# Kernel tuning notes

Measured on AMD Instinct MI355X. Metric: run time of the kernel, lower is better.

## Reference

```python
import jax, jax.numpy as jnp
import numpy as np

B, N, DIM = 4, 2048, 1024
H, DH = 16, 64


def setup_inputs() -> dict:
    key = jax.random.key(0)
    k1, k2, k3 = jax.random.split(key, 3)
    x = jax.random.normal(k1, (B, N, DIM), dtype=jnp.float32)
    # nn.Linear weight layout: [out_features, in_features]; y = x @ W.T
    w_qkv = jax.random.normal(k2, (3 * H * DH, DIM), dtype=jnp.float32) * (DIM ** -0.5)
    w_out = jax.random.normal(k3, (DIM, H * DH), dtype=jnp.float32) * ((H * DH) ** -0.5)
    b_out = jnp.zeros((DIM,), dtype=jnp.float32)
    return {"x": x, "w_qkv": w_qkv, "w_out": w_out, "b_out": b_out}


def reference(x, w_qkv, w_out, b_out):
    scale = DH ** -0.5
    qkv = jnp.einsum('bnd,ed->bne', x, w_qkv)            # [B,N,3*H*DH]
    q, k, v = jnp.split(qkv, 3, axis=-1)
    def to_heads(t):
        return t.reshape(B, N, H, DH).transpose(0, 2, 1, 3)  # b h n d
    q, k, v = to_heads(q), to_heads(k), to_heads(v)
    scores = jnp.einsum('bhnd,bhmd->bhnm', q, k) * scale  # [B,H,N,N]
    att = jax.nn.softmax(scores, axis=-1)
    out = jnp.einsum('bhnm,bhmd->bhnd', att, v)
    out = out.transpose(0, 2, 1, 3).reshape(B, N, H * DH)  # b n (h d)
    return jnp.einsum('bne,de->bnd', out, w_out) + b_out
```

## Files before the change

kernel.cpp:

```cpp
#include <hip/hip_runtime.h>
#include <hip/hip_bf16.h>
#include <math.h>

#define B_   4
#define N_   2048
#define DIM_ 1024
#define H_   16
#define DH_  64
#define E3_  3072

typedef __attribute__((ext_vector_type(8)))  short s8v;
typedef __attribute__((ext_vector_type(4)))  float f4v;
typedef __attribute__((ext_vector_type(16))) float f16v;

__device__ __forceinline__ unsigned short f2bf_fast(float f) {
    return (unsigned short)((__builtin_bit_cast(unsigned int, f) + 0x8000u) >> 16);
}
__device__ __forceinline__ unsigned int pkbf(float a, float b) {
    unsigned int ua = __builtin_bit_cast(unsigned int, a) + 0x8000u;
    unsigned int ub = __builtin_bit_cast(unsigned int, b) + 0x8000u;
    return __builtin_amdgcn_perm(ub, ua, 0x07060302);
}
__device__ __forceinline__ unsigned int cvtpk(float a, float b) {
    unsigned int r;
    asm("v_cvt_pk_bf16_f32 %0, %1, %2" : "=v"(r) : "v"(a), "v"(b));
    return r;
}
__device__ __forceinline__ uint2 pl32(unsigned int a, unsigned int b) {
    asm volatile("v_permlane32_swap_b32 %0, %1" : "+v"(a), "+v"(b));
    return make_uint2(a, b);
}

__device__ __forceinline__ void gload_lds16(const void* g, void* l) {
    __builtin_amdgcn_global_load_lds(
        (const __attribute__((address_space(1))) unsigned int*)(uintptr_t)g,
        (__attribute__((address_space(3))) unsigned int*)(uintptr_t)l,
        16, 0, 0);
}

__global__ __launch_bounds__(256) void cvt_bf16(
    const float* __restrict__ in, unsigned short* __restrict__ out, int n)
{
    const int i = (blockIdx.x * 256 + threadIdx.x) * 4;
    if (i < n) {
        float4 v = *(const float4*)(in + i);
        uint2 pk;
        pk.x = pkbf(v.x, v.y);
        pk.y = pkbf(v.z, v.w);
        *(uint2*)(out + i) = pk;
    }
}

__global__ __launch_bounds__(512, 1) void gemm_qkv(
    const unsigned short* __restrict__ A,
    const unsigned short* __restrict__ Bw,
    unsigned short* __restrict__ Cb,
    unsigned short* __restrict__ Vt)
{
    __shared__ unsigned short Ls[2][28672];

    const int tid  = threadIdx.x;
    const int w    = tid >> 6;
    const int lane = tid & 63;
    const int quad = lane >> 4;
    const int l15  = lane & 15;
    const int wm   = w & 1;
    const int wn   = w >> 1;

    const int lin = blockIdx.y * 16 + blockIdx.x;
    const int swz = (lin & 7) * 64 + (lin >> 3);
    const int m0  = (swz >> 4) * 256;
    const int n0  = (swz & 15) * 192;

    const int r8  = lane >> 3;
    const int chk = (lane & 7) ^ r8;

    f4v acc[8][3];
    #pragma unroll
    for (int i = 0; i < 8; i++)
        #pragma unroll
        for (int j = 0; j < 3; j++) acc[i][j] = (f4v){0.f, 0.f, 0.f, 0.f};

    #pragma unroll
    for (int j = 0; j < 7; j++) {
        const int u = w * 7 + j;
        const unsigned short* src = (u < 32)
            ? A  + (size_t)(m0 + u * 8 + r8) * 1024 + chk * 8
            : Bw + (size_t)(n0 + (u - 32) * 8 + r8) * 1024 + chk * 8;
        gload_lds16(src, &Ls[0][u * 512]);
    }
    __syncthreads();

    for (int t = 0; t < 16; t++) {
        const int cur = t & 1;

        if (t + 1 < 16) {
            const int k0 = (t + 1) * 64;
            #pragma unroll
            for (int j = 0; j < 7; j++) {
                const int u = w * 7 + j;
                const unsigned short* src = (u < 32)
                    ? A  + (size_t)(m0 + u * 8 + r8) * 1024 + k0 + chk * 8
                    : Bw + (size_t)(n0 + (u - 32) * 8 + r8) * 1024 + k0 + chk * 8;
                gload_lds16(src, &Ls[cur ^ 1][u * 512]);
            }
        }

        #pragma unroll
        for (int s = 0; s < 2; s++) {
            s8v af[8], bf[3];
            #pragma unroll
            for (int ms = 0; ms < 8; ms++) {
                const int row = wm * 128 + ms * 16 + l15;
                af[ms] = *(const s8v*)&Ls[cur][row * 64 + (((s * 4 + quad) ^ (l15 & 7)) * 8)];
            }
            #pragma unroll
            for (int ns = 0; ns < 3; ns++) {
                const int row = 256 + wn * 48 + ns * 16 + l15;
                bf[ns] = *(const s8v*)&Ls[cur][row * 64 + (((s * 4 + quad) ^ (l15 & 7)) * 8)];
            }
            __builtin_amdgcn_s_setprio(1);
            #pragma unroll
            for (int ms = 0; ms < 8; ms++)
                #pragma unroll
                for (int ns = 0; ns < 3; ns++)
                    acc[ms][ns] = __builtin_amdgcn_mfma_f32_16x16x32_bf16(
                        af[ms], bf[ns], acc[ms][ns], 0, 0, 0);
            __builtin_amdgcn_s_setprio(0);
        }

        __syncthreads();
    }

    #pragma unroll
    for (int ns = 0; ns < 3; ns++) {
        const int colb = n0 + wn * 48 + ns * 16;
        if (colb < 2048) {
            const float mul = (colb < 1024) ? 0.18033688011112042f : 1.0f;
            #pragma unroll
            for (int ms = 0; ms < 8; ms++)
                #pragma unroll
                for (int r = 0; r < 4; r++) {
                    const int row = m0 + wm * 128 + ms * 16 + quad * 4 + r;
                    Cb[(size_t)row * E3_ + colb + l15] = f2bf_fast(acc[ms][ns][r] * mul);
                }
        } else {
            const int e = colb + l15 - 2048;
            const int hh = e >> 6, d = e & 63;
            #pragma unroll
            for (int ms = 0; ms < 8; ms++) {
                const int row = m0 + wm * 128 + ms * 16 + quad * 4;
                const int bb = row >> 11, nn = row & 2047;
                uint2 pk;
                pk.x = pkbf(acc[ms][ns][0], acc[ms][ns][1]);
                pk.y = pkbf(acc[ms][ns][2], acc[ms][ns][3]);
                *(uint2*)&Vt[(((size_t)bb * 16 + hh) * 64 + d) * 2048 + nn] = pk;
            }
        }
    }
}

__global__ __launch_bounds__(256) void gemm_out(
    const unsigned short* __restrict__ A,
    const unsigned short* __restrict__ Bw,
    const float* __restrict__ bias,
    float* __restrict__ Cf,
    int M, int Nc, int K)
{
    __shared__ unsigned short As[128 * 32];
    __shared__ unsigned short Bs[128 * 32];

    const int tid  = threadIdx.x;
    const int w    = tid >> 6;
    const int lane = tid & 63;
    const int quad = lane >> 4;
    const int l15  = lane & 15;
    const int wm   = w & 1, wn = w >> 1;

    const int nwx = gridDim.x;
    const int lin = blockIdx.y * nwx + blockIdx.x;
    const int cpx = (nwx * gridDim.y) >> 3;
    const int swz = (lin & 7) * cpx + (lin >> 3);
    const int m0  = (swz / nwx) * 128, n0 = (swz % nwx) * 128;

    const int srow = lane >> 2;
    const int sch  = (lane & 3) * 8;

    f4v acc[4][4];
    #pragma unroll
    for (int i = 0; i < 4; i++)
        #pragma unroll
        for (int j = 0; j < 4; j++) acc[i][j] = (f4v){0.f, 0.f, 0.f, 0.f};

    for (int k0 = 0; k0 < K; k0 += 32) {
        __syncthreads();
        #pragma unroll
        for (int i = 0; i < 2; i++) {
            const int rbase = w * 32 + i * 16;
            gload_lds16(A  + (size_t)(m0 + rbase + srow) * K + k0 + sch,
                        &As[rbase * 32]);
            gload_lds16(Bw + (size_t)(n0 + rbase + srow) * K + k0 + sch,
                        &Bs[rbase * 32]);
        }
        __syncthreads();

        s8v af[4], bf[4];
        #pragma unroll
        for (int i = 0; i < 4; i++) {
            af[i] = *(const s8v*)&As[(wm * 64 + i * 16 + l15) * 32 + quad * 8];
            bf[i] = *(const s8v*)&Bs[(wn * 64 + i * 16 + l15) * 32 + quad * 8];
        }
        #pragma unroll
        for (int ms = 0; ms < 4; ms++)
            #pragma unroll
            for (int ns = 0; ns < 4; ns++)
                acc[ms][ns] = __builtin_amdgcn_mfma_f32_16x16x32_bf16(
                    af[ms], bf[ns], acc[ms][ns], 0, 0, 0);
    }

    #pragma unroll
    for (int ns = 0; ns < 4; ns++) {
        const float bz = bias[n0 + wn * 64 + ns * 16 + l15];
        #pragma unroll
        for (int ms = 0; ms < 4; ms++)
            #pragma unroll
            for (int r = 0; r < 4; r++) {
                const int row = m0 + wm * 64 + ms * 16 + quad * 4 + r;
                Cf[(size_t)row * Nc + n0 + wn * 64 + ns * 16 + l15] =
                    acc[ms][ns][r] + bz;
            }
    }
}

__global__ __launch_bounds__(512, 4) void attn_mfma(
    const unsigned short* __restrict__ qkv,
    const unsigned short* __restrict__ vT,
    unsigned short* __restrict__ ao)
{
    __shared__ __align__(16) unsigned short Ks[2][64][64];
    __shared__ __align__(16) unsigned short Vs[2][64][64];

    const int tid  = threadIdx.x;
    const int w    = tid >> 6;
    const int lane = tid & 63;
    const int l31  = lane & 31;
    const int hi5  = lane >> 5;
    const int h8   = hi5 * 8;

    const int lin = blockIdx.y * 8 + blockIdx.x;
    const int swz = (lin & 7) * 64 + (lin >> 3);
    const int bx  = swz & 7;
    const int bh  = swz >> 3;
    const int b   = bh >> 4;
    const int h   = bh & 15;
    const int q0  = bx * 256;
    const int qb  = q0 + w * 32;

    const unsigned short* qp  = qkv + (size_t)b * N_ * E3_ + (size_t)h * DH_;
    const unsigned short* kp  = qp + 1024;
    const unsigned short* vtp = vT + (size_t)bh * 64 * 2048;

    const int drow = lane >> 3;
    const int dchk = (lane & 7) ^ drow;
    const int grow = w * 8 + drow;

    s8v bq[4];
    {
        const unsigned short* qrow = qp + (size_t)(qb + l31) * E3_;
        #pragma unroll
        for (int ks = 0; ks < 4; ks++)
            bq[ks] = *(const s8v*)(qrow + ks * 16 + h8);
    }

    s8v ones;
    #pragma unroll
    for (int i = 0; i < 8; i++) ones[i] = (short)0x3F80;

    const f16v fzero = {0.f,0.f,0.f,0.f,0.f,0.f,0.f,0.f,
                        0.f,0.f,0.f,0.f,0.f,0.f,0.f,0.f};
    f16v o0 = fzero, o1 = fzero;
    f16v lc = fzero;

    gload_lds16(kp  + (size_t)grow * E3_  + dchk * 8, &Ks[0][w * 8][0]);
    gload_lds16(vtp + (size_t)grow * 2048 + dchk * 8, &Vs[0][w * 8][0]);
    __syncthreads();

    for (int kt = 0; kt < N_ / 64; kt++) {
        const int cur = kt & 1;

        if (kt + 1 < N_ / 64) {
            const int kn = (kt + 1) * 64;
            gload_lds16(kp  + (size_t)(kn + grow) * E3_  + dchk * 8,
                        &Ks[cur ^ 1][w * 8][0]);
            gload_lds16(vtp + (size_t)grow * 2048 + kn + dchk * 8,
                        &Vs[cur ^ 1][w * 8][0]);
        }

        #pragma unroll
        for (int ksub = 0; ksub < 2; ksub++) {
            const int krow = ksub * 32 + l31;
            const int ksw  = (l31 & 7) * 8;
            s8v ak[4];
            #pragma unroll
            for (int ks = 0; ks < 4; ks++)
                ak[ks] = *(const s8v*)&Ks[cur][krow][(ks * 16 + h8) ^ ksw];

            f16v st = fzero;
            __builtin_amdgcn_s_setprio(1);
            st = __builtin_amdgcn_mfma_f32_32x32x16_bf16(ak[0], bq[0], st, 0, 0, 0);
            st = __builtin_amdgcn_mfma_f32_32x32x16_bf16(ak[1], bq[1], st, 0, 0, 0);
            st = __builtin_amdgcn_mfma_f32_32x32x16_bf16(ak[2], bq[2], st, 0, 0, 0);
            st = __builtin_amdgcn_mfma_f32_32x32x16_bf16(ak[3], bq[3], st, 0, 0, 0);
            __builtin_amdgcn_s_setprio(0);

            float pe[16];
            #pragma unroll
            for (int i = 0; i < 16; i++)
                pe[i] = __builtin_amdgcn_exp2f(st[i]);

            s8v pa[2];
            {
                union { s8v v; unsigned int u[4]; } f0, f1;
                uint2 r;
                r = pl32(cvtpk(pe[0],  pe[1]),  cvtpk(pe[4],  pe[5]));
                f0.u[0] = r.x; f0.u[2] = r.y;
                r = pl32(cvtpk(pe[2],  pe[3]),  cvtpk(pe[6],  pe[7]));
                f0.u[1] = r.x; f0.u[3] = r.y;
                r = pl32(cvtpk(pe[8],  pe[9]),  cvtpk(pe[12], pe[13]));
                f1.u[0] = r.x; f1.u[2] = r.y;
                r = pl32(cvtpk(pe[10], pe[11]), cvtpk(pe[14], pe[15]));
                f1.u[1] = r.x; f1.u[3] = r.y;
                pa[0] = f0.v;
                pa[1] = f1.v;
            }

            #pragma unroll
            for (int j = 0; j < 2; j++) {
                const int kbase = (ksub * 2 + j) * 16 + h8;
                const int vsw   = (l31 & 7) * 8;
                s8v bv0 = *(const s8v*)&Vs[cur][l31     ][kbase ^ vsw];
                s8v bv1 = *(const s8v*)&Vs[cur][32 + l31][kbase ^ vsw];
                __builtin_amdgcn_s_setprio(1);
                o0 = __builtin_amdgcn_mfma_f32_32x32x16_bf16(pa[j], bv0, o0, 0, 0, 0);
                o1 = __builtin_amdgcn_mfma_f32_32x32x16_bf16(pa[j], bv1, o1, 0, 0, 0);
                lc = __builtin_amdgcn_mfma_f32_32x32x16_bf16(pa[j], ones, lc, 0, 0, 0);
                __builtin_amdgcn_s_setprio(0);
            }
        }

        __syncthreads();
    }

    {
        float inv[16];
        #pragma unroll
        for (int r = 0; r < 16; r++) inv[r] = 1.f / lc[r];
        #pragma unroll
        for (int r = 0; r < 16; r++) {
            const int qrow = qb + (r & 3) + 8 * (r >> 2) + 4 * hi5;
            const size_t base = ((size_t)b * N_ + qrow) * (H_ * DH_) + h * DH_;
            ao[base + l31]      = f2bf_fast(o0[r] * inv[r]);
            ao[base + 32 + l31] = f2bf_fast(o1[r] * inv[r]);
        }
    }
}

extern "C" void kernel_launch(void* const* d_in, const int* in_sizes, int n_in,
                              void* d_out, int out_size, void* d_ws, size_t ws_size,
                              hipStream_t stream) {
    const float* x     = (const float*)d_in[0];
    const float* w_qkv = (const float*)d_in[1];
    const float* w_out = (const float*)d_in[2];
    const float* b_out = (const float*)d_in[3];
    float* out = (float*)d_out;

    char* ws = (char*)d_ws;
    unsigned short* x_bf    = (unsigned short*)(ws);
    unsigned short* wqkv_bf = (unsigned short*)(ws + (((size_t)16) << 20));
    unsigned short* wout_bf = (unsigned short*)(ws + (((size_t)22) << 20));
    unsigned short* qkv_bf  = (unsigned short*)(ws + (((size_t)24) << 20));
    unsigned short* vT      = (unsigned short*)(ws + (((size_t)72) << 20));
    unsigned short* ao_bf   = (unsigned short*)(ws + (((size_t)88) << 20));

    const int M = B_ * N_;

    cvt_bf16<<<(M * DIM_) / 1024, 256, 0, stream>>>(x, x_bf, M * DIM_);
    cvt_bf16<<<(E3_ * DIM_) / 1024, 256, 0, stream>>>(w_qkv, wqkv_bf, E3_ * DIM_);
    cvt_bf16<<<(DIM_ * DIM_) / 1024, 256, 0, stream>>>(w_out, wout_bf, DIM_ * DIM_);

    {
        dim3 grid(E3_ / 192, M / 256);
        gemm_qkv<<<grid, 512, 0, stream>>>(x_bf, wqkv_bf, qkv_bf, vT);
    }
    {
        dim3 grid(N_ / 256, B_ * H_);
        attn_mfma<<<grid, 512, 0, stream>>>(qkv_bf, vT, ao_bf);
    }
    {
        dim3 grid(DIM_ / 128, M / 128);
        gemm_out<<<grid, 256, 0, stream>>>(ao_bf, wout_bf, b_out,
                                           out, M, DIM_, DIM_);
    }
    (void)in_sizes; (void)n_in; (void)out_size; (void)ws_size;
}
```

Baseline: 257.7 us.

## Process two query sub-tiles per wave in attention to reuse K/V fragments

Each wave now handles 64 query rows (two 32-row sub-tiles) instead of 32, so every K and V fragment read from LDS feeds twice as many MFMAs. Each block covers 512 queries, the grid is halved, the block swizzle is adjusted, and launch bounds drop to 2 blocks per CU to allow more registers. This cuts LDS reads and global K/V tile loads per unit of work. The cost is higher register pressure, lower occupancy, and fewer blocks (256) to spread across the CUs.

```diff
diff --git a/kernel.cpp b/kernel.cpp
--- a/kernel.cpp
+++ b/kernel.cpp
@@ -232,7 +232,7 @@
     }
 }
 
-__global__ __launch_bounds__(512, 4) void attn_mfma(
+__global__ __launch_bounds__(512, 2) void attn_mfma(
     const unsigned short* __restrict__ qkv,
     const unsigned short* __restrict__ vT,
     unsigned short* __restrict__ ao)
@@ -247,14 +247,13 @@
     const int hi5  = lane >> 5;
     const int h8   = hi5 * 8;
 
-    const int lin = blockIdx.y * 8 + blockIdx.x;
-    const int swz = (lin & 7) * 64 + (lin >> 3);
-    const int bx  = swz & 7;
-    const int bh  = swz >> 3;
+    const int lin = blockIdx.y * 4 + blockIdx.x;
+    const int j0  = (lin & 7) * 32 + (lin >> 3);
+    const int bx  = j0 & 3;
+    const int bh  = j0 >> 2;
     const int b   = bh >> 4;
     const int h   = bh & 15;
-    const int q0  = bx * 256;
-    const int qb  = q0 + w * 32;
+    const int qb  = bx * 512 + w * 64;
 
     const unsigned short* qp  = qkv + (size_t)b * N_ * E3_ + (size_t)h * DH_;
     const unsigned short* kp  = qp + 1024;
@@ -264,12 +263,13 @@
     const int dchk = (lane & 7) ^ drow;
     const int grow = w * 8 + drow;
 
-    s8v bq[4];
-    {
-        const unsigned short* qrow = qp + (size_t)(qb + l31) * E3_;
+    s8v bq[2][4];
+    #pragma unroll
+    for (int sub = 0; sub < 2; sub++) {
+        const unsigned short* qrow = qp + (size_t)(qb + sub * 32 + l31) * E3_;
         #pragma unroll
         for (int ks = 0; ks < 4; ks++)
-            bq[ks] = *(const s8v*)(qrow + ks * 16 + h8);
+            bq[sub][ks] = *(const s8v*)(qrow + ks * 16 + h8);
     }
 
     s8v ones;
@@ -278,8 +278,10 @@
 
     const f16v fzero = {0.f,0.f,0.f,0.f,0.f,0.f,0.f,0.f,
                         0.f,0.f,0.f,0.f,0.f,0.f,0.f,0.f};
-    f16v o0 = fzero, o1 = fzero;
-    f16v lc = fzero;
+    f16v o[2][2];
+    o[0][0] = fzero; o[0][1] = fzero; o[1][0] = fzero; o[1][1] = fzero;
+    f16v lc[2];
+    lc[0] = fzero; lc[1] = fzero;
 
     gload_lds16(kp  + (size_t)grow * E3_  + dchk * 8, &Ks[0][w * 8][0]);
     gload_lds16(vtp + (size_t)grow * 2048 + dchk * 8, &Vs[0][w * 8][0]);
@@ -305,21 +307,22 @@
             for (int ks = 0; ks < 4; ks++)
                 ak[ks] = *(const s8v*)&Ks[cur][krow][(ks * 16 + h8) ^ ksw];
 
-            f16v st = fzero;
-            __builtin_amdgcn_s_setprio(1);
-            st = __builtin_amdgcn_mfma_f32_32x32x16_bf16(ak[0], bq[0], st, 0, 0, 0);
-            st = __builtin_amdgcn_mfma_f32_32x32x16_bf16(ak[1], bq[1], st, 0, 0, 0);
-            st = __builtin_amdgcn_mfma_f32_32x32x16_bf16(ak[2], bq[2], st, 0, 0, 0);
-            st = __builtin_amdgcn_mfma_f32_32x32x16_bf16(ak[3], bq[3], st, 0, 0, 0);
-            __builtin_amdgcn_s_setprio(0);
-
-            float pe[16];
-            #pragma unroll
-            for (int i = 0; i < 16; i++)
-                pe[i] = __builtin_amdgcn_exp2f(st[i]);
-
-            s8v pa[2];
-            {
+            s8v pa[2][2];
+            #pragma unroll
+            for (int sub = 0; sub < 2; sub++) {
+                f16v st = fzero;
+                __builtin_amdgcn_s_setprio(1);
+                st = __builtin_amdgcn_mfma_f32_32x32x16_bf16(ak[0], bq[sub][0], st, 0, 0, 0);
+                st = __builtin_amdgcn_mfma_f32_32x32x16_bf16(ak[1], bq[sub][1], st, 0, 0, 0);
+                st = __builtin_amdgcn_mfma_f32_32x32x16_bf16(ak[2], bq[sub][2], st, 0, 0, 0);
+                st = __builtin_amdgcn_mfma_f32_32x32x16_bf16(ak[3], bq[sub][3], st, 0, 0, 0);
+                __builtin_amdgcn_s_setprio(0);
+
+                float pe[16];
+                #pragma unroll
+                for (int i = 0; i < 16; i++)
+                    pe[i] = __builtin_amdgcn_exp2f(st[i]);
+
                 union { s8v v; unsigned int u[4]; } f0, f1;
                 uint2 r;
                 r = pl32(cvtpk(pe[0],  pe[1]),  cvtpk(pe[4],  pe[5]));
@@ -330,8 +333,8 @@
                 f1.u[0] = r.x; f1.u[2] = r.y;
                 r = pl32(cvtpk(pe[10], pe[11]), cvtpk(pe[14], pe[15]));
                 f1.u[1] = r.x; f1.u[3] = r.y;
-                pa[0] = f0.v;
-                pa[1] = f1.v;
+                pa[sub][0] = f0.v;
+                pa[sub][1] = f1.v;
             }
 
             #pragma unroll
@@ -341,9 +344,12 @@
                 s8v bv0 = *(const s8v*)&Vs[cur][l31     ][kbase ^ vsw];
                 s8v bv1 = *(const s8v*)&Vs[cur][32 + l31][kbase ^ vsw];
                 __builtin_amdgcn_s_setprio(1);
-                o0 = __builtin_amdgcn_mfma_f32_32x32x16_bf16(pa[j], bv0, o0, 0, 0, 0);
-                o1 = __builtin_amdgcn_mfma_f32_32x32x16_bf16(pa[j], bv1, o1, 0, 0, 0);
-                lc = __builtin_amdgcn_mfma_f32_32x32x16_bf16(pa[j], ones, lc, 0, 0, 0);
+                o[0][0] = __builtin_amdgcn_mfma_f32_32x32x16_bf16(pa[0][j], bv0, o[0][0], 0, 0, 0);
+                o[0][1] = __builtin_amdgcn_mfma_f32_32x32x16_bf16(pa[0][j], bv1, o[0][1], 0, 0, 0);
+                o[1][0] = __builtin_amdgcn_mfma_f32_32x32x16_bf16(pa[1][j], bv0, o[1][0], 0, 0, 0);
+                o[1][1] = __builtin_amdgcn_mfma_f32_32x32x16_bf16(pa[1][j], bv1, o[1][1], 0, 0, 0);
+                lc[0]   = __builtin_amdgcn_mfma_f32_32x32x16_bf16(pa[0][j], ones, lc[0], 0, 0, 0);
+                lc[1]   = __builtin_amdgcn_mfma_f32_32x32x16_bf16(pa[1][j], ones, lc[1], 0, 0, 0);
                 __builtin_amdgcn_s_setprio(0);
             }
         }
@@ -351,16 +357,18 @@
         __syncthreads();
     }
 
-    {
+    #pragma unroll
+    for (int sub = 0; sub < 2; sub++) {
         float inv[16];
         #pragma unroll
-        for (int r = 0; r < 16; r++) inv[r] = 1.f / lc[r];
+        for (int r = 0; r < 16; r++) inv[r] = 1.f / lc[sub][r];
         #pragma unroll
         for (int r = 0; r < 16; r++) {
-            const int qrow = qb + (r & 3) + 8 * (r >> 2) + 4 * hi5;
+            const int crow = (r & 3) + 8 * (r >> 2) + 4 * hi5;
+            const int qrow = qb + sub * 32 + crow;
             const size_t base = ((size_t)b * N_ + qrow) * (H_ * DH_) + h * DH_;
-            ao[base + l31]      = f2bf_fast(o0[r] * inv[r]);
-            ao[base + 32 + l31] = f2bf_fast(o1[r] * inv[r]);
+            ao[base + l31]      = f2bf_fast(o[sub][0][r] * inv[r]);
+            ao[base + 32 + l31] = f2bf_fast(o[sub][1][r] * inv[r]);
         }
     }
 }
@@ -393,7 +401,7 @@
         gemm_qkv<<<grid, 512, 0, stream>>>(x_bf, wqkv_bf, qkv_bf, vT);
     }
     {
-        dim3 grid(N_ / 256, B_ * H_);
+        dim3 grid(N_ / 512, B_ * H_);
         attn_mfma<<<grid, 512, 0, stream>>>(qkv_bf, vT, ao_bf);
     }
     {
```

After: 254.3 us. About the same (-1.3%).

## Double-buffer and swizzle the output GEMM, and fuse the bf16 conversion launches

Applied to the files above, without the earlier changes.

The output-projection GEMM now uses a K-tile of 64 with two LDS buffers, so the next tile's global-to-LDS load overlaps the current tile's MFMAs. It also XOR-swizzles the LDS chunks to avoid bank conflicts and raises wave priority around the MFMA block. The three fp32-to-bf16 conversion launches are merged into one kernel to cut launch overhead. Shapes are now hardcoded, and the larger LDS footprint may limit how many blocks fit per CU.

```diff
diff --git a/kernel.cpp b/kernel.cpp
--- a/kernel.cpp
+++ b/kernel.cpp
@@ -38,17 +38,23 @@
         16, 0, 0);
 }
 
-__global__ __launch_bounds__(256) void cvt_bf16(
-    const float* __restrict__ in, unsigned short* __restrict__ out, int n)
+__global__ __launch_bounds__(256) void cvt_all(
+    const float* __restrict__ x,  const float* __restrict__ wq,
+    const float* __restrict__ wo,
+    unsigned short* __restrict__ xb, unsigned short* __restrict__ wqb,
+    unsigned short* __restrict__ wob)
 {
-    const int i = (blockIdx.x * 256 + threadIdx.x) * 4;
-    if (i < n) {
-        float4 v = *(const float4*)(in + i);
-        uint2 pk;
-        pk.x = pkbf(v.x, v.y);
-        pk.y = pkbf(v.z, v.w);
-        *(uint2*)(out + i) = pk;
-    }
+    const int bid = blockIdx.x;
+    const float* in; unsigned short* out; int rb;
+    if (bid < 8192)       { in = x;  out = xb;  rb = bid; }
+    else if (bid < 11264) { in = wq; out = wqb; rb = bid - 8192; }
+    else                  { in = wo; out = wob; rb = bid - 11264; }
+    const int i = (rb * 256 + threadIdx.x) * 4;
+    float4 v = *(const float4*)(in + i);
+    uint2 pk;
+    pk.x = pkbf(v.x, v.y);
+    pk.y = pkbf(v.z, v.w);
+    *(uint2*)(out + i) = pk;
 }
 
 __global__ __launch_bounds__(512, 1) void gemm_qkv(
@@ -160,31 +166,29 @@
     }
 }
 
-__global__ __launch_bounds__(256) void gemm_out(
+__global__ __launch_bounds__(256, 2) void gemm_out(
     const unsigned short* __restrict__ A,
     const unsigned short* __restrict__ Bw,
     const float* __restrict__ bias,
-    float* __restrict__ Cf,
-    int M, int Nc, int K)
+    float* __restrict__ Cf)
 {
-    __shared__ unsigned short As[128 * 32];
-    __shared__ unsigned short Bs[128 * 32];
+    __shared__ unsigned short Ls[2][16384];
 
     const int tid  = threadIdx.x;
     const int w    = tid >> 6;
     const int lane = tid & 63;
     const int quad = lane >> 4;
     const int l15  = lane & 15;
-    const int wm   = w & 1, wn = w >> 1;
-
-    const int nwx = gridDim.x;
-    const int lin = blockIdx.y * nwx + blockIdx.x;
-    const int cpx = (nwx * gridDim.y) >> 3;
-    const int swz = (lin & 7) * cpx + (lin >> 3);
-    const int m0  = (swz / nwx) * 128, n0 = (swz % nwx) * 128;
-
-    const int srow = lane >> 2;
-    const int sch  = (lane & 3) * 8;
+    const int wm   = w & 1;
+    const int wn   = w >> 1;
+
+    const int lin = blockIdx.y * 8 + blockIdx.x;
+    const int swz = (lin & 7) * 64 + (lin >> 3);
+    const int m0  = (swz >> 3) * 128;
+    const int n0  = (swz & 7) * 128;
+
+    const int r8  = lane >> 3;
+    const int chk = (lane & 7) ^ r8;
 
     f4v acc[4][4];
     #pragma unroll
@@ -192,30 +196,55 @@
         #pragma unroll
         for (int j = 0; j < 4; j++) acc[i][j] = (f4v){0.f, 0.f, 0.f, 0.f};
 
-    for (int k0 = 0; k0 < K; k0 += 32) {
+    #pragma unroll
+    for (int j = 0; j < 8; j++) {
+        const int u = w * 8 + j;
+        const unsigned short* src = (u < 16)
+            ? A  + (size_t)(m0 + u * 8 + r8) * 1024 + chk * 8
+            : Bw + (size_t)(n0 + (u - 16) * 8 + r8) * 1024 + chk * 8;
+        gload_lds16(src, &Ls[0][u * 512]);
+    }
+    __syncthreads();
+
+    for (int t = 0; t < 16; t++) {
+        const int cur = t & 1;
+
+        if (t + 1 < 16) {
+            const int k0 = (t + 1) * 64;
+            #pragma unroll
+            for (int j = 0; j < 8; j++) {
+                const int u = w * 8 + j;
+                const unsigned short* src = (u < 16)
+                    ? A  + (size_t)(m0 + u * 8 + r8) * 1024 + k0 + chk * 8
+                    : Bw + (size_t)(n0 + (u - 16) * 8 + r8) * 1024 + k0 + chk * 8;
+                gload_lds16(src, &Ls[cur ^ 1][u * 512]);
+            }
+        }
+
+        #pragma unroll
+        for (int s = 0; s < 2; s++) {
+            s8v af[4], bf[4];
+            #pragma unroll
+            for (int ms = 0; ms < 4; ms++) {
+                const int row = wm * 64 + ms * 16 + l15;
+                af[ms] = *(const s8v*)&Ls[cur][row * 64 + (((s * 4 + quad) ^ (l15 & 7)) * 8)];
+            }
+            #pragma unroll
+            for (int ns = 0; ns < 4; ns++) {
+                const int row = 128 + wn * 64 + ns * 16 + l15;
+                bf[ns] = *(const s8v*)&Ls[cur][row * 64 + (((s * 4 + quad) ^ (l15 & 7)) * 8)];
+            }
+            __builtin_amdgcn_s_setprio(1);
+            #pragma unroll
+            for (int ms = 0; ms < 4; ms++)
+                #pragma unroll
+                for (int ns = 0; ns < 4; ns++)
+                    acc[ms][ns] = __builtin_amdgcn_mfma_f32_16x16x32_bf16(
+                        af[ms], bf[ns], acc[ms][ns], 0, 0, 0);
+            __builtin_amdgcn_s_setprio(0);
+        }
+
         __syncthreads();
-        #pragma unroll
-        for (int i = 0; i < 2; i++) {
-            const int rbase = w * 32 + i * 16;
-            gload_lds16(A  + (size_t)(m0 + rbase + srow) * K + k0 + sch,
-                        &As[rbase * 32]);
-            gload_lds16(Bw + (size_t)(n0 + rbase + srow) * K + k0 + sch,
-                        &Bs[rbase * 32]);
-        }
-        __syncthreads();
-
-        s8v af[4], bf[4];
-        #pragma unroll
-        for (int i = 0; i < 4; i++) {
-            af[i] = *(const s8v*)&As[(wm * 64 + i * 16 + l15) * 32 + quad * 8];
-            bf[i] = *(const s8v*)&Bs[(wn * 64 + i * 16 + l15) * 32 + quad * 8];
-        }
-        #pragma unroll
-        for (int ms = 0; ms < 4; ms++)
-            #pragma unroll
-            for (int ns = 0; ns < 4; ns++)
-                acc[ms][ns] = __builtin_amdgcn_mfma_f32_16x16x32_bf16(
-                    af[ms], bf[ns], acc[ms][ns], 0, 0, 0);
     }
 
     #pragma unroll
@@ -226,7 +255,7 @@
             #pragma unroll
             for (int r = 0; r < 4; r++) {
                 const int row = m0 + wm * 64 + ms * 16 + quad * 4 + r;
-                Cf[(size_t)row * Nc + n0 + wn * 64 + ns * 16 + l15] =
+                Cf[(size_t)row * 1024 + n0 + wn * 64 + ns * 16 + l15] =
                     acc[ms][ns][r] + bz;
             }
     }
@@ -384,9 +413,7 @@
 
     const int M = B_ * N_;
 
-    cvt_bf16<<<(M * DIM_) / 1024, 256, 0, stream>>>(x, x_bf, M * DIM_);
-    cvt_bf16<<<(E3_ * DIM_) / 1024, 256, 0, stream>>>(w_qkv, wqkv_bf, E3_ * DIM_);
-    cvt_bf16<<<(DIM_ * DIM_) / 1024, 256, 0, stream>>>(w_out, wout_bf, DIM_ * DIM_);
+    cvt_all<<<12288, 256, 0, stream>>>(x, w_qkv, w_out, x_bf, wqkv_bf, wout_bf);
 
     {
         dim3 grid(E3_ / 192, M / 256);
@@ -398,8 +425,7 @@
     }
     {
         dim3 grid(DIM_ / 128, M / 128);
-        gemm_out<<<grid, 256, 0, stream>>>(ao_bf, wout_bf, b_out,
-                                           out, M, DIM_, DIM_);
+        gemm_out<<<grid, 256, 0, stream>>>(ao_bf, wout_bf, b_out, out);
     }
     (void)in_sizes; (void)n_in; (void)out_size; (void)ws_size;
 }
```

New measurement: 250.1 us, median of 2. -3.0%, faster.
